# Kernel optimization log

Hardware: AMD Instinct MI355X
Metric: run time of the kernel (lower is better)

The kernel has to match this reference:

```python
import jax, jax.numpy as jnp
import numpy as np

DIM = 1024
HEADS = 16
DIM_HEAD = 64
INNER = HEADS * DIM_HEAD  # 1024


def setup_inputs() -> dict:
    key = jax.random.key(0)
    ks = jax.random.split(key, 5)
    x = jax.random.normal(ks[0], (4, 2048, DIM), dtype=jnp.float32)
    ln_g = jnp.ones((DIM,), dtype=jnp.float32)
    ln_b = jnp.zeros((DIM,), dtype=jnp.float32)
    w_qkv = jax.random.normal(ks[1], (DIM, 3 * INNER), dtype=jnp.float32) / np.sqrt(DIM)
    w_out = jax.random.normal(ks[2], (INNER, DIM), dtype=jnp.float32) / np.sqrt(INNER)
    b_out = jax.random.normal(ks[3], (DIM,), dtype=jnp.float32) * 0.01
    return {"x": x, "ln_g": ln_g, "ln_b": ln_b, "w_qkv": w_qkv, "w_out": w_out, "b_out": b_out}


def reference(x, ln_g, ln_b, w_qkv, w_out, b_out):
    eps = 1e-5  # torch nn.LayerNorm default
    mu = jnp.mean(x, axis=-1, keepdims=True)
    var = jnp.mean(jnp.square(x - mu), axis=-1, keepdims=True)
    xn = (x - mu) / jnp.sqrt(var + eps) * ln_g + ln_b

    qkv = xn @ w_qkv  # [b, n, 3*inner]
    q, k, v = jnp.split(qkv, 3, axis=-1)
    b, n, _ = q.shape
    q = q.reshape(b, n, HEADS, DIM_HEAD).transpose(0, 2, 1, 3)  # b h n d
    k = k.reshape(b, n, HEADS, DIM_HEAD).transpose(0, 2, 1, 3)
    v = v.reshape(b, n, HEADS, DIM_HEAD).transpose(0, 2, 1, 3)

    scale = DIM_HEAD ** -0.5
    sim = jnp.einsum('bhid,bhjd->bhij', q * scale, k)
    attn = jax.nn.softmax(sim, axis=-1)  # max-subtracted internally, matches detach'd amax trick
    out = jnp.einsum('bhij,bhjd->bhid', attn, v)
    out = out.transpose(0, 2, 1, 3).reshape(b, n, INNER)
    return out @ w_out + b_out
```

## Files before the change

kernel.cpp:

```cpp
#include <hip/hip_runtime.h>
#include <hip/hip_bf16.h>

#define DIM 1024
#define SEQ 2048
#define BATCH 4
#define HEADS 16
#define DHEAD 64
#define ROWS (BATCH * SEQ)
#define QKV_N (3 * DIM)

typedef __attribute__((ext_vector_type(4))) float f32x4;
typedef __attribute__((ext_vector_type(8))) short s16x8;

__device__ __forceinline__ unsigned short f2bf(float f) {
  union { __hip_bfloat16 h; unsigned short u; } c;
  c.h = __float2bfloat16(f);
  return c.u;
}

__device__ __forceinline__ unsigned cvtpk(float a, float b) {
  unsigned r;
  asm("v_cvt_pk_bf16_f32 %0, %1, %2" : "=v"(r) : "v"(a), "v"(b));
  return r;
}

__device__ __forceinline__ void gl_lds16(const void* g, void* l) {
  __builtin_amdgcn_global_load_lds(
      (const __attribute__((address_space(1))) unsigned int*)g,
      (__attribute__((address_space(3))) unsigned int*)l, 16, 0, 0);
}

__global__ __launch_bounds__(256) void ln_bf16(const float* __restrict__ x,
                                               const float* __restrict__ g,
                                               const float* __restrict__ beta,
                                               unsigned short* __restrict__ xn) {
  const int row = blockIdx.x;
  const int tid = threadIdx.x;
  float4 v = ((const float4*)(x + (size_t)row * DIM))[tid];
  float s  = v.x + v.y + v.z + v.w;
  float ss = v.x * v.x + v.y * v.y + v.z * v.z + v.w * v.w;
#pragma unroll
  for (int off = 32; off > 0; off >>= 1) {
    s  += __shfl_down(s, off);
    ss += __shfl_down(ss, off);
  }
  __shared__ float red[8];
  const int wid = tid >> 6;
  if ((tid & 63) == 0) { red[wid] = s; red[4 + wid] = ss; }
  __syncthreads();
  if (tid == 0) {
    red[0] = red[0] + red[1] + red[2] + red[3];
    red[4] = red[4] + red[5] + red[6] + red[7];
  }
  __syncthreads();
  const float mu   = red[0] * (1.0f / DIM);
  const float var  = red[4] * (1.0f / DIM) - mu * mu;
  const float rstd = rsqrtf(var + 1e-5f);
  float4 gg = ((const float4*)g)[tid];
  float4 bb = ((const float4*)beta)[tid];
  ushort4 o;
  o.x = f2bf((v.x - mu) * rstd * gg.x + bb.x);
  o.y = f2bf((v.y - mu) * rstd * gg.y + bb.y);
  o.z = f2bf((v.z - mu) * rstd * gg.z + bb.z);
  o.w = f2bf((v.w - mu) * rstd * gg.w + bb.w);
  ((ushort4*)(xn + (size_t)row * DIM))[tid] = o;
}

__global__ __launch_bounds__(256) void transpose_w(const float* __restrict__ W,
                                                   unsigned short* __restrict__ Wt,
                                                   int Kd, int Nd,
                                                   int qcols, float qscale) {
  __shared__ float T[64][65];
  const int t = threadIdx.x;
  const int n0 = blockIdx.x * 64, k0 = blockIdx.y * 64;
#pragma unroll
  for (int r = 0; r < 4; r++) {
    int gidx = t + r * 256;
    int row = gidx >> 4, c4 = (gidx & 15) << 2;
    float4 v = *(const float4*)(W + (size_t)(k0 + row) * Nd + n0 + c4);
    T[row][c4 + 0] = v.x; T[row][c4 + 1] = v.y;
    T[row][c4 + 2] = v.z; T[row][c4 + 3] = v.w;
  }
  __syncthreads();
#pragma unroll
  for (int r = 0; r < 2; r++) {
    int gidx = t + r * 256;
    int nrow = gidx >> 3, cs = (gidx & 7) << 3;
    float sc = (n0 + nrow < qcols) ? qscale : 1.0f;
    s16x8 o;
#pragma unroll
    for (int j = 0; j < 8; j++) o[j] = (short)f2bf(T[cs + j][nrow] * sc);
    *(s16x8*)(Wt + (size_t)(n0 + nrow) * Kd + k0 + cs) = o;
  }
}

__global__ __launch_bounds__(256) void transpose_v(const unsigned short* __restrict__ qkv,
                                                   unsigned short* __restrict__ vt) {
  __shared__ unsigned short T[64][72];
  const int t = threadIdx.x;
  const int s0 = blockIdx.x * 64;
  const int bh = blockIdx.y, b = bh >> 4, h = bh & 15;
#pragma unroll
  for (int r = 0; r < 2; r++) {
    int g = t + r * 256;
    int row = g >> 3, c = (g & 7) << 3;
    s16x8 v = *(const s16x8*)(qkv + ((size_t)(b * SEQ + s0 + row)) * QKV_N + 2 * DIM + h * DHEAD + c);
    *(s16x8*)(&T[row][c]) = v;
  }
  __syncthreads();
#pragma unroll
  for (int r = 0; r < 2; r++) {
    int g = t + r * 256;
    int drow = g >> 3, sc = (g & 7) << 3;
    s16x8 o;
#pragma unroll
    for (int j = 0; j < 8; j++) o[j] = (short)T[sc + j][drow];
    *(s16x8*)(vt + ((size_t)(bh * DHEAD + drow)) * SEQ + s0 + sc) = o;
  }
}

template <bool OUT_BF16, bool BIAS>
__global__ __launch_bounds__(256) void gemm_bt_bf16(const unsigned short* __restrict__ A,
                                                    const unsigned short* __restrict__ Bt,
                                                    const float* __restrict__ bias,
                                                    void* __restrict__ Cv,
                                                    int M, int N, int K) {
  __shared__ unsigned short As[2][128 * 32];
  __shared__ unsigned short Bs[2][128 * 32];
  const int tid = threadIdx.x;
  const int w = tid >> 6, l = tid & 63;
  const int lr = l & 15, lg = l >> 4;
  const int wr = w >> 1, wc = w & 1;

  const int nbx = N >> 7;
  const int nwg = nbx * (M >> 7);
  int bid = blockIdx.y * nbx + blockIdx.x;
  int swz = (bid & 7) * (nwg >> 3) + (bid >> 3);
  const int bx = swz % nbx, by = swz / nbx;
  const int m0 = by << 7, n0 = bx << 7;

  auto stage = [&](int k0, int buf) {
#pragma unroll
    for (int c = 0; c < 2; c++) {
      int gidx = tid + c * 256;
      int row = gidx >> 2, sl = gidx & 3;
      int ss = sl ^ ((row ^ (row >> 2)) & 3);
      gl_lds16(A  + (size_t)(m0 + row) * K + k0 + ss * 8, &As[buf][gidx * 8]);
      gl_lds16(Bt + (size_t)(n0 + row) * K + k0 + ss * 8, &Bs[buf][gidx * 8]);
    }
  };

  f32x4 acc[4][4];
#pragma unroll
  for (int mi = 0; mi < 4; mi++)
#pragma unroll
    for (int ni = 0; ni < 4; ni++) acc[mi][ni] = (f32x4){0.f, 0.f, 0.f, 0.f};

  const int NT = K >> 5;
  stage(0, 0);
  int cur = 0;
  for (int t = 0; t < NT; t++) {
    __syncthreads();
    if (t + 1 < NT) stage((t + 1) << 5, cur ^ 1);
    s16x8 af[4], bfr[4];
#pragma unroll
    for (int mi = 0; mi < 4; mi++) {
      int rowa = wr * 64 + mi * 16 + lr;
      int sla = lg ^ ((rowa ^ (rowa >> 2)) & 3);
      af[mi] = *(const s16x8*)&As[cur][rowa * 32 + sla * 8];
      int rowb = wc * 64 + mi * 16 + lr;
      int slb = lg ^ ((rowb ^ (rowb >> 2)) & 3);
      bfr[mi] = *(const s16x8*)&Bs[cur][rowb * 32 + slb * 8];
    }
#pragma unroll
    for (int mi = 0; mi < 4; mi++)
#pragma unroll
      for (int ni = 0; ni < 4; ni++)
        acc[mi][ni] = __builtin_amdgcn_mfma_f32_16x16x32_bf16(af[mi], bfr[ni], acc[mi][ni], 0, 0, 0);
    cur ^= 1;
  }

#pragma unroll
  for (int mi = 0; mi < 4; mi++) {
#pragma unroll
    for (int ni = 0; ni < 4; ni++) {
      int col = n0 + wc * 64 + ni * 16 + lr;
      float bv = BIAS ? bias[col] : 0.f;
#pragma unroll
      for (int i = 0; i < 4; i++) {
        size_t rowg = (size_t)m0 + wr * 64 + mi * 16 + lg * 4 + i;
        float vv = acc[mi][ni][i] + bv;
        if (OUT_BF16) ((unsigned short*)Cv)[rowg * N + col] = f2bf(vv);
        else          ((float*)Cv)[rowg * N + col] = vv;
      }
    }
  }
}

__global__ __launch_bounds__(256) void attn_mfma(const unsigned short* __restrict__ qkv,
                                                 const unsigned short* __restrict__ vt,
                                                 unsigned short* __restrict__ aout) {
  __shared__ unsigned short Qs[128 * 64];
  __shared__ unsigned short Ks[2][64 * 64];
  __shared__ unsigned short Vs[2][64 * 64];
  __shared__ unsigned short Ps[4][32 * 68];
  const int tid = threadIdx.x;
  const int w = tid >> 6, l = tid & 63;
  const int lr = l & 15, lg = l >> 4;
  const int qt = blockIdx.x, bh = blockIdx.y;
  const int b = bh >> 4, h = bh & 15;
  const size_t qrow0 = (size_t)b * SEQ + qt * 128;

  auto stageKV = [&](int t, int buf) {
#pragma unroll
    for (int c = 0; c < 2; c++) {
      int gidx = tid + c * 256;
      int row = gidx >> 3, sl = gidx & 7;
      int ss = sl ^ (row & 7);
      gl_lds16(qkv + ((size_t)b * SEQ + t * 64 + row) * QKV_N + DIM + h * DHEAD + ss * 8,
               &Ks[buf][gidx * 8]);
      gl_lds16(vt + ((size_t)bh * DHEAD + row) * SEQ + t * 64 + ss * 8,
               &Vs[buf][gidx * 8]);
    }
  };

#pragma unroll
  for (int c = 0; c < 4; c++) {
    int gidx = tid + c * 256;
    int row = gidx >> 3, sl = gidx & 7;
    int ss = sl ^ (row & 7);
    gl_lds16(qkv + (qrow0 + row) * QKV_N + h * DHEAD + ss * 8, &Qs[gidx * 8]);
  }
  stageKV(0, 0);
  __syncthreads();

  s16x8 qf[2][2];
#pragma unroll
  for (int rf = 0; rf < 2; rf++)
#pragma unroll
    for (int s = 0; s < 2; s++) {
      int row = w * 32 + rf * 16 + lr;
      int sl = (s * 4 + lg) ^ (lr & 7);
      qf[rf][s] = *(const s16x8*)&Qs[row * 64 + sl * 8];
    }

  float lsum0 = 0.f, lsum1 = 0.f;
  f32x4 of[2][4];
#pragma unroll
  for (int rf = 0; rf < 2; rf++)
#pragma unroll
    for (int ni = 0; ni < 4; ni++) of[rf][ni] = (f32x4){0.f, 0.f, 0.f, 0.f};

  int cur = 0;
  const int NT = SEQ / 64;
  for (int t = 0; t < NT; t++) {
    if (t + 1 < NT) stageKV(t + 1, cur ^ 1);

    f32x4 stf[2][4];
    __builtin_amdgcn_s_setprio(1);
#pragma unroll
    for (int ni = 0; ni < 4; ni++) {
      int row = ni * 16 + lr;
      s16x8 k0 = *(const s16x8*)&Ks[cur][row * 64 + ((lg) ^ (lr & 7)) * 8];
      s16x8 k1 = *(const s16x8*)&Ks[cur][row * 64 + ((4 + lg) ^ (lr & 7)) * 8];
      stf[0][ni] = __builtin_amdgcn_mfma_f32_16x16x32_bf16(k0, qf[0][0], (f32x4){0.f, 0.f, 0.f, 0.f}, 0, 0, 0);
      stf[1][ni] = __builtin_amdgcn_mfma_f32_16x16x32_bf16(k0, qf[1][0], (f32x4){0.f, 0.f, 0.f, 0.f}, 0, 0, 0);
      stf[0][ni] = __builtin_amdgcn_mfma_f32_16x16x32_bf16(k1, qf[0][1], stf[0][ni], 0, 0, 0);
      stf[1][ni] = __builtin_amdgcn_mfma_f32_16x16x32_bf16(k1, qf[1][1], stf[1][ni], 0, 0, 0);
    }
    __builtin_amdgcn_s_setprio(0);

#pragma unroll
    for (int ni = 0; ni < 4; ni++)
#pragma unroll
      for (int i = 0; i < 4; i++) {
        float p0 = exp2f(stf[0][ni][i]);
        float p1 = exp2f(stf[1][ni][i]);
        stf[0][ni][i] = p0; lsum0 += p0;
        stf[1][ni][i] = p1; lsum1 += p1;
      }

#pragma unroll
    for (int rf = 0; rf < 2; rf++)
#pragma unroll
      for (int ni = 0; ni < 4; ni++) {
        uint2 pw;
        pw.x = cvtpk(stf[rf][ni][0], stf[rf][ni][1]);
        pw.y = cvtpk(stf[rf][ni][2], stf[rf][ni][3]);
        int sl = (ni * 4 + lg) ^ ((lr & 7) << 1);
        *(uint2*)&Ps[w][(rf * 16 + lr) * 68 + sl * 4] = pw;
      }

    s16x8 pf[2][2];
#pragma unroll
    for (int rf = 0; rf < 2; rf++)
#pragma unroll
      for (int ks = 0; ks < 2; ks++) {
        int sl0 = (ks * 8 + lg * 2) ^ ((lr & 7) << 1);
        int base = (rf * 16 + lr) * 68;
        uint2 pa = *(const uint2*)&Ps[w][base + sl0 * 4];
        uint2 pb = *(const uint2*)&Ps[w][base + (sl0 + 1) * 4];
        union { unsigned u[4]; s16x8 v; } U;
        U.u[0] = pa.x; U.u[1] = pa.y; U.u[2] = pb.x; U.u[3] = pb.y;
        pf[rf][ks] = U.v;
      }

    __builtin_amdgcn_s_setprio(1);
#pragma unroll
    for (int ni = 0; ni < 4; ni++) {
      int row = ni * 16 + lr;
      s16x8 v0 = *(const s16x8*)&Vs[cur][row * 64 + ((lg) ^ (lr & 7)) * 8];
      s16x8 v1 = *(const s16x8*)&Vs[cur][row * 64 + ((4 + lg) ^ (lr & 7)) * 8];
      of[0][ni] = __builtin_amdgcn_mfma_f32_16x16x32_bf16(v0, pf[0][0], of[0][ni], 0, 0, 0);
      of[1][ni] = __builtin_amdgcn_mfma_f32_16x16x32_bf16(v0, pf[1][0], of[1][ni], 0, 0, 0);
      of[0][ni] = __builtin_amdgcn_mfma_f32_16x16x32_bf16(v1, pf[0][1], of[0][ni], 0, 0, 0);
      of[1][ni] = __builtin_amdgcn_mfma_f32_16x16x32_bf16(v1, pf[1][1], of[1][ni], 0, 0, 0);
    }
    __builtin_amdgcn_s_setprio(0);
    __syncthreads();
    cur ^= 1;
  }

  lsum0 += __shfl_xor(lsum0, 16);
  lsum0 += __shfl_xor(lsum0, 32);
  lsum1 += __shfl_xor(lsum1, 16);
  lsum1 += __shfl_xor(lsum1, 32);

#pragma unroll
  for (int rf = 0; rf < 2; rf++) {
    float inv = 1.0f / (rf ? lsum1 : lsum0);
    size_t rowg = qrow0 + w * 32 + rf * 16 + lr;
#pragma unroll
    for (int ni = 0; ni < 4; ni++) {
      uint2 ov;
      ov.x = cvtpk(of[rf][ni][0] * inv, of[rf][ni][1] * inv);
      ov.y = cvtpk(of[rf][ni][2] * inv, of[rf][ni][3] * inv);
      *(uint2*)&aout[rowg * DIM + h * DHEAD + ni * 16 + lg * 4] = ov;
    }
  }
}

extern "C" void kernel_launch(void* const* d_in, const int* in_sizes, int n_in,
                              void* d_out, int out_size, void* d_ws, size_t ws_size,
                              hipStream_t stream) {
  const float* x     = (const float*)d_in[0];
  const float* ln_g  = (const float*)d_in[1];
  const float* ln_b  = (const float*)d_in[2];
  const float* w_qkv = (const float*)d_in[3];
  const float* w_out = (const float*)d_in[4];
  const float* b_out = (const float*)d_in[5];
  float* outp = (float*)d_out;

  char* ws = (char*)d_ws;
  unsigned short* xn      = (unsigned short*)(ws);
  unsigned short* qkv     = (unsigned short*)(ws + (16ull << 20));
  unsigned short* vtb     = (unsigned short*)(ws + (64ull << 20));
  unsigned short* aout    = (unsigned short*)(ws + (80ull << 20));
  unsigned short* wt_qkv  = (unsigned short*)(ws + (96ull << 20));
  unsigned short* wt_out  = (unsigned short*)(ws + (104ull << 20));

  const float CEXP = 0.18033688011112042f;

  ln_bf16<<<ROWS, 256, 0, stream>>>(x, ln_g, ln_b, xn);
  transpose_w<<<dim3(QKV_N / 64, DIM / 64), 256, 0, stream>>>(w_qkv, wt_qkv, DIM, QKV_N, DIM, CEXP);
  transpose_w<<<dim3(DIM / 64, DIM / 64), 256, 0, stream>>>(w_out, wt_out, DIM, DIM, 0, 1.0f);
  gemm_bt_bf16<true, false><<<dim3(QKV_N / 128, ROWS / 128), 256, 0, stream>>>(
      xn, wt_qkv, nullptr, qkv, ROWS, QKV_N, DIM);
  transpose_v<<<dim3(SEQ / 64, BATCH * HEADS), 256, 0, stream>>>(qkv, vtb);
  attn_mfma<<<dim3(SEQ / 128, BATCH * HEADS), 256, 0, stream>>>(qkv, vtb, aout);
  gemm_bt_bf16<false, true><<<dim3(DIM / 128, ROWS / 128), 256, 0, stream>>>(
      aout, wt_out, b_out, outp, ROWS, DIM, DIM);
}
```

Baseline: 327.5 us.

## Load attention K/V fragments directly from global into registers, dropping LDS staging

The attention kernel no longer stages Q, K and V tiles through shared memory with block-wide barriers. Each wave now loads its MFMA fragments straight from global (L2-cached) memory into registers, double-buffering K fragments across an unrolled pair of tiles and loading V just in time. A block-index swizzle groups blocks sharing the same batch-head to improve L2 locality. This removes LDS traffic and the per-tile __syncthreads, but every wave now re-reads K/V from global/L2, four times the traffic per block, and register pressure rises.

```diff
diff --git a/kernel.cpp b/kernel.cpp
--- a/kernel.cpp
+++ b/kernel.cpp
@@ -200,49 +200,37 @@
 __global__ __launch_bounds__(256) void attn_mfma(const unsigned short* __restrict__ qkv,
                                                  const unsigned short* __restrict__ vt,
                                                  unsigned short* __restrict__ aout) {
-  __shared__ unsigned short Qs[128 * 64];
-  __shared__ unsigned short Ks[2][64 * 64];
-  __shared__ unsigned short Vs[2][64 * 64];
   __shared__ unsigned short Ps[4][32 * 68];
   const int tid = threadIdx.x;
   const int w = tid >> 6, l = tid & 63;
   const int lr = l & 15, lg = l >> 4;
-  const int qt = blockIdx.x, bh = blockIdx.y;
+  const int bid = blockIdx.y * (SEQ / 128) + blockIdx.x;
+  const int swz = (bid & 7) * 128 + (bid >> 3);
+  const int qt = swz & 15, bh = swz >> 4;
   const int b = bh >> 4, h = bh & 15;
   const size_t qrow0 = (size_t)b * SEQ + qt * 128;
 
-  auto stageKV = [&](int t, int buf) {
-#pragma unroll
-    for (int c = 0; c < 2; c++) {
-      int gidx = tid + c * 256;
-      int row = gidx >> 3, sl = gidx & 7;
-      int ss = sl ^ (row & 7);
-      gl_lds16(qkv + ((size_t)b * SEQ + t * 64 + row) * QKV_N + DIM + h * DHEAD + ss * 8,
-               &Ks[buf][gidx * 8]);
-      gl_lds16(vt + ((size_t)bh * DHEAD + row) * SEQ + t * 64 + ss * 8,
-               &Vs[buf][gidx * 8]);
-    }
-  };
-
-#pragma unroll
-  for (int c = 0; c < 4; c++) {
-    int gidx = tid + c * 256;
-    int row = gidx >> 3, sl = gidx & 7;
-    int ss = sl ^ (row & 7);
-    gl_lds16(qkv + (qrow0 + row) * QKV_N + h * DHEAD + ss * 8, &Qs[gidx * 8]);
-  }
-  stageKV(0, 0);
-  __syncthreads();
+  const unsigned short* kb = qkv + ((size_t)b * SEQ) * QKV_N + DIM + h * DHEAD;
+  const unsigned short* vb = vt + (size_t)bh * DHEAD * SEQ;
+  const int kvo = lr * QKV_N + lg * 8;
+  const int vvo = lr * SEQ + lg * 8;
 
   s16x8 qf[2][2];
-#pragma unroll
-  for (int rf = 0; rf < 2; rf++)
-#pragma unroll
-    for (int s = 0; s < 2; s++) {
-      int row = w * 32 + rf * 16 + lr;
-      int sl = (s * 4 + lg) ^ (lr & 7);
-      qf[rf][s] = *(const s16x8*)&Qs[row * 64 + sl * 8];
-    }
+  {
+    const unsigned short* qb = qkv + (qrow0 + (size_t)w * 32) * QKV_N + h * DHEAD;
+#pragma unroll
+    for (int rf = 0; rf < 2; rf++)
+#pragma unroll
+      for (int s = 0; s < 2; s++)
+        qf[rf][s] = *(const s16x8*)(qb + (rf * 16 + lr) * QKV_N + s * 32 + lg * 8);
+  }
+
+  s16x8 kfA[4][2], kfB[4][2];
+#pragma unroll
+  for (int ni = 0; ni < 4; ni++)
+#pragma unroll
+    for (int kk = 0; kk < 2; kk++)
+      kfA[ni][kk] = *(const s16x8*)(kb + kvo + ni * 16 * QKV_N + kk * 32);
 
   float lsum0 = 0.f, lsum1 = 0.f;
   f32x4 of[2][4];
@@ -251,24 +239,37 @@
 #pragma unroll
     for (int ni = 0; ni < 4; ni++) of[rf][ni] = (f32x4){0.f, 0.f, 0.f, 0.f};
 
-  int cur = 0;
   const int NT = SEQ / 64;
-  for (int t = 0; t < NT; t++) {
-    if (t + 1 < NT) stageKV(t + 1, cur ^ 1);
-
+
+  auto tile = [&](int t, s16x8 (&kc)[4][2], s16x8 (&kn)[4][2]) {
     f32x4 stf[2][4];
     __builtin_amdgcn_s_setprio(1);
 #pragma unroll
     for (int ni = 0; ni < 4; ni++) {
-      int row = ni * 16 + lr;
-      s16x8 k0 = *(const s16x8*)&Ks[cur][row * 64 + ((lg) ^ (lr & 7)) * 8];
-      s16x8 k1 = *(const s16x8*)&Ks[cur][row * 64 + ((4 + lg) ^ (lr & 7)) * 8];
-      stf[0][ni] = __builtin_amdgcn_mfma_f32_16x16x32_bf16(k0, qf[0][0], (f32x4){0.f, 0.f, 0.f, 0.f}, 0, 0, 0);
-      stf[1][ni] = __builtin_amdgcn_mfma_f32_16x16x32_bf16(k0, qf[1][0], (f32x4){0.f, 0.f, 0.f, 0.f}, 0, 0, 0);
-      stf[0][ni] = __builtin_amdgcn_mfma_f32_16x16x32_bf16(k1, qf[0][1], stf[0][ni], 0, 0, 0);
-      stf[1][ni] = __builtin_amdgcn_mfma_f32_16x16x32_bf16(k1, qf[1][1], stf[1][ni], 0, 0, 0);
+      stf[0][ni] = __builtin_amdgcn_mfma_f32_16x16x32_bf16(kc[ni][0], qf[0][0], (f32x4){0.f, 0.f, 0.f, 0.f}, 0, 0, 0);
+      stf[1][ni] = __builtin_amdgcn_mfma_f32_16x16x32_bf16(kc[ni][0], qf[1][0], (f32x4){0.f, 0.f, 0.f, 0.f}, 0, 0, 0);
+      stf[0][ni] = __builtin_amdgcn_mfma_f32_16x16x32_bf16(kc[ni][1], qf[0][1], stf[0][ni], 0, 0, 0);
+      stf[1][ni] = __builtin_amdgcn_mfma_f32_16x16x32_bf16(kc[ni][1], qf[1][1], stf[1][ni], 0, 0, 0);
     }
     __builtin_amdgcn_s_setprio(0);
+
+    s16x8 vf[4][2];
+    {
+      const unsigned short* vbt = vb + t * 64;
+#pragma unroll
+      for (int ni = 0; ni < 4; ni++)
+#pragma unroll
+        for (int ks = 0; ks < 2; ks++)
+          vf[ni][ks] = *(const s16x8*)(vbt + vvo + ni * 16 * SEQ + ks * 32);
+    }
+    if (t + 1 < NT) {
+      const unsigned short* kbt = kb + (size_t)(t + 1) * 64 * QKV_N;
+#pragma unroll
+      for (int ni = 0; ni < 4; ni++)
+#pragma unroll
+        for (int kk = 0; kk < 2; kk++)
+          kn[ni][kk] = *(const s16x8*)(kbt + kvo + ni * 16 * QKV_N + kk * 32);
+    }
 
 #pragma unroll
     for (int ni = 0; ni < 4; ni++)
@@ -308,17 +309,17 @@
     __builtin_amdgcn_s_setprio(1);
 #pragma unroll
     for (int ni = 0; ni < 4; ni++) {
-      int row = ni * 16 + lr;
-      s16x8 v0 = *(const s16x8*)&Vs[cur][row * 64 + ((lg) ^ (lr & 7)) * 8];
-      s16x8 v1 = *(const s16x8*)&Vs[cur][row * 64 + ((4 + lg) ^ (lr & 7)) * 8];
-      of[0][ni] = __builtin_amdgcn_mfma_f32_16x16x32_bf16(v0, pf[0][0], of[0][ni], 0, 0, 0);
-      of[1][ni] = __builtin_amdgcn_mfma_f32_16x16x32_bf16(v0, pf[1][0], of[1][ni], 0, 0, 0);
-      of[0][ni] = __builtin_amdgcn_mfma_f32_16x16x32_bf16(v1, pf[0][1], of[0][ni], 0, 0, 0);
-      of[1][ni] = __builtin_amdgcn_mfma_f32_16x16x32_bf16(v1, pf[1][1], of[1][ni], 0, 0, 0);
+      of[0][ni] = __builtin_amdgcn_mfma_f32_16x16x32_bf16(vf[ni][0], pf[0][0], of[0][ni], 0, 0, 0);
+      of[1][ni] = __builtin_amdgcn_mfma_f32_16x16x32_bf16(vf[ni][0], pf[1][0], of[1][ni], 0, 0, 0);
+      of[0][ni] = __builtin_amdgcn_mfma_f32_16x16x32_bf16(vf[ni][1], pf[0][1], of[0][ni], 0, 0, 0);
+      of[1][ni] = __builtin_amdgcn_mfma_f32_16x16x32_bf16(vf[ni][1], pf[1][1], of[1][ni], 0, 0, 0);
     }
     __builtin_amdgcn_s_setprio(0);
-    __syncthreads();
-    cur ^= 1;
+  };
+
+  for (int t = 0; t < NT; t += 2) {
+    tile(t, kfA, kfB);
+    tile(t + 1, kfB, kfA);
   }
 
   lsum0 += __shfl_xor(lsum0, 16);
```

Result: slower. 438.0 us (+33.7%).
